# Performance work log

Hardware: AMD Instinct MI355X
Metric: run time of the kernel (lower is better)

The kernel has to match this reference:

```python
import jax, jax.numpy as jnp
import numpy as np

EPS = 1e-8

def setup_inputs() -> dict:
    key = jax.random.key(0)
    k1, k2 = jax.random.split(key)
    B, IN, OUT, G = 32768, 256, 256, 5
    x = jax.random.normal(k1, (B, IN), dtype=jnp.float32)
    grid = jnp.linspace(-1.0, 1.0, G).astype(jnp.float32)
    coef = jax.random.normal(k2, (OUT, IN, G), dtype=jnp.float32) * 0.1
    scale = jnp.ones((OUT, IN), dtype=jnp.float32)
    bias = jnp.zeros((OUT,), dtype=jnp.float32)
    return {"x": x, "grid": grid, "coef": coef, "scale": scale, "bias": bias}

def reference(x, grid, coef, scale, bias):
    # global min-max normalization to [-1, 1]
    xmin, xmax = x.min(), x.max()
    xn = 2.0 * (x - xmin) / (xmax - xmin + EPS) - 1.0
    # cubic bump B-spline-like basis: (batch, in, grid)
    dist = jnp.abs(xn[..., None] - grid)
    basis = jnp.where(dist < 1.0, 1.0 - dist ** 3, 0.0)
    basis = basis / (basis.sum(axis=-1, keepdims=True) + EPS)
    # fused contraction over (in, grid); equals ((basis*coef).sum(-1)*scale).sum(-1)
    w = coef * scale[..., None]          # (out, in, grid)
    out = jnp.einsum('big,oig->bo', basis, w) + bias
    return out
```

## Files before the change

### kernel.cpp

```cpp
#include <hip/hip_runtime.h>
#include <stdint.h>


#define B_SZ   32768
#define IN_SZ  256
#define OUT_SZ 256
#define EPSF   1e-8f

typedef __bf16 bf16x8 __attribute__((ext_vector_type(8)));
typedef unsigned short ushort8 __attribute__((ext_vector_type(8)));
typedef float floatx16 __attribute__((ext_vector_type(16)));

union frag_u { uint4 u; bf16x8 v; };

__device__ __forceinline__ unsigned short f2bf(float f) {
  unsigned u = __float_as_uint(f);
  u += 0x7FFFu + ((u >> 16) & 1u);
  return (unsigned short)(u >> 16);
}


__global__ void __launch_bounds__(256) prep_kernel(const float* __restrict__ coef,
                                                   const float* __restrict__ scale,
                                                   const float* __restrict__ x,
                                                   unsigned short* __restrict__ wf,
                                                   float* __restrict__ part, int n4) {
  const int t = threadIdx.x;
  if (blockIdx.x < 256) {
    int idx = blockIdx.x * 256 + t;
    int o = idx >> 8, i = idx & 255;
    float s = scale[idx];
    const float* c = coef + (size_t)idx * 5;
    ushort8 v;
    v[0] = f2bf(c[0] * s); v[1] = f2bf(c[1] * s); v[2] = f2bf(c[2] * s);
    v[3] = f2bf(c[3] * s); v[4] = f2bf(c[4] * s);
    v[5] = 0; v[6] = 0; v[7] = 0;
    int chunk = (((o >> 5) * 64 + (i >> 2)) * 2 + ((i >> 1) & 1)) * 64
                + (i & 1) * 32 + (o & 31);
    *(ushort8*)(wf + (size_t)chunk * 8) = v;
  } else {
    int mb = blockIdx.x - 256;
    const float4* x4 = (const float4*)x;
    float lmin = 1e30f, lmax = -1e30f;
    for (int i = mb * 256 + t; i < n4; i += 256 * 256) {
      float4 v = x4[i];
      lmin = fminf(lmin, fminf(fminf(v.x, v.y), fminf(v.z, v.w)));
      lmax = fmaxf(lmax, fmaxf(fmaxf(v.x, v.y), fmaxf(v.z, v.w)));
    }
    #pragma unroll
    for (int off = 32; off >= 1; off >>= 1) {
      lmin = fminf(lmin, __shfl_down(lmin, off, 64));
      lmax = fmaxf(lmax, __shfl_down(lmax, off, 64));
    }
    __shared__ float smn[4], smx[4];
    if ((t & 63) == 0) { smn[t >> 6] = lmin; smx[t >> 6] = lmax; }
    __syncthreads();
    if (t == 0) {
      part[2 * mb]     = fminf(fminf(smn[0], smn[1]), fminf(smn[2], smn[3]));
      part[2 * mb + 1] = fmaxf(fmaxf(smx[0], smx[1]), fmaxf(smx[2], smx[3]));
    }
  }
}

__device__ __forceinline__ bf16x8 basisfrag(float xval, float scA, float scB) {
  float xn = fmaf(xval, scA, scB);
  float d0 = xn + 1.0f, d1 = xn + 0.5f, d3 = xn - 0.5f, d4 = xn - 1.0f;
  float b0 = fmaxf(fmaf(d0 * d0, -fabsf(d0), 1.0f), 0.0f);
  float b1 = fmaxf(fmaf(d1 * d1, -fabsf(d1), 1.0f), 0.0f);
  float b2 = fmaxf(fmaf(xn * xn, -fabsf(xn), 1.0f), 0.0f);
  float b3 = fmaxf(fmaf(d3 * d3, -fabsf(d3), 1.0f), 0.0f);
  float b4 = fmaxf(fmaf(d4 * d4, -fabsf(d4), 1.0f), 0.0f);
  float sum = ((b0 + b1) + (b2 + b3)) + b4;
  float inv = __builtin_amdgcn_rcpf(sum);
  b0 *= inv; b1 *= inv; b2 *= inv; b3 *= inv; b4 *= inv;
  frag_u r;
  r.u.x = __builtin_amdgcn_perm(__float_as_uint(b1), __float_as_uint(b0), 0x07060302u);
  r.u.y = __builtin_amdgcn_perm(__float_as_uint(b3), __float_as_uint(b2), 0x07060302u);
  r.u.z = __float_as_uint(b4) >> 16;
  r.u.w = 0u;
  return r.v;
}

__global__ void __launch_bounds__(256, 2) kan_gemm(
    const float* __restrict__ x,
    const unsigned short* __restrict__ wf,
    const float* __restrict__ bias,
    const float* __restrict__ part,
    float* __restrict__ out)
{
  __shared__ __align__(16) unsigned short Bb[2][16384];
  __shared__ float2 red[4];

  const int t = threadIdx.x;
  const int lane = t & 63;
  const int wm = t >> 6;
  const int l31 = lane & 31, lh = lane >> 5;
  const int bRow = blockIdx.x * 128;
  const int bCol = blockIdx.y * 128;
  const int row = bRow + wm * 32 + l31;

  auto stage = [&](int c, int buf) {
    #pragma unroll
    for (int r = 0; r < 8; ++r) {
      int idx = r * 4 + wm;
      const unsigned short* src = wf +
          ((size_t)(((blockIdx.y * 4 + (idx >> 3)) * 64 + (c * 4 + ((idx >> 1) & 3))) * 2
                    + (idx & 1))) * 512 + (size_t)lane * 8;
      __builtin_amdgcn_global_load_lds(
          (const __attribute__((address_space(1))) unsigned int*)src,
          (__attribute__((address_space(3))) unsigned int*)(&Bb[buf][idx * 512 + lane * 8]),
          16, 0, 0);
    }
  };

  const float* xrow = x + (size_t)row * IN_SZ;

  stage(0, 0);
  float4 xq[4], xqn[4];
  #pragma unroll
  for (int g = 0; g < 4; ++g) xq[g] = *(const float4*)(xrow + g * 4);

  float2 p = ((const float2*)part)[t];
  float mn = p.x, mx = p.y;
  #pragma unroll
  for (int off = 32; off >= 1; off >>= 1) {
    mn = fminf(mn, __shfl_down(mn, off, 64));
    mx = fmaxf(mx, __shfl_down(mx, off, 64));
  }
  if (lane == 0) red[wm] = make_float2(mn, mx);
  __syncthreads();
  mn = fminf(fminf(red[0].x, red[1].x), fminf(red[2].x, red[3].x));
  mx = fmaxf(fmaxf(red[0].y, red[1].y), fmaxf(red[2].y, red[3].y));
  const float scA = 2.0f / (mx - mn + EPSF);
  const float scB = -mn * scA - 1.0f;

  floatx16 acc[4] = {};
  bf16x8 br[2][8];

  auto ldsB = [&](int ktr, int buf, bf16x8* dst) {
    #pragma unroll
    for (int q = 0; q < 8; ++q) {
      int ni = q >> 1, ks = q & 1;
      dst[q] = *(const bf16x8*)(&Bb[buf][((ni * 4 + ktr) * 2 + ks) * 512 + lane * 8]);
    }
  };

  for (int c = 0; c < 16; ++c) {
    const int buf = c & 1;

    if (c < 15) {
      #pragma unroll
      for (int g = 0; g < 4; ++g)
        xqn[g] = *(const float4*)(xrow + (c + 1) * 16 + g * 4);
      stage(c + 1, buf ^ 1);
      __builtin_amdgcn_sched_barrier(0);
      asm volatile("s_waitcnt vmcnt(12)\n\ts_barrier" ::: "memory");
    } else {
      asm volatile("s_waitcnt vmcnt(0)\n\ts_barrier" ::: "memory");
    }

    ldsB(0, buf, br[0]);

    #pragma unroll
    for (int ktr = 0; ktr < 4; ++ktr) {
      if (ktr < 3) ldsB(ktr + 1, buf, br[(ktr + 1) & 1]);

      float xv0 = lh ? xq[ktr].y : xq[ktr].x;
      float xv1 = lh ? xq[ktr].w : xq[ktr].z;
      bf16x8 af0 = basisfrag(xv0, scA, scB);
      bf16x8 af1 = basisfrag(xv1, scA, scB);

      bf16x8* B = br[ktr & 1];
      __builtin_amdgcn_s_setprio(1);
      #pragma unroll
      for (int ni = 0; ni < 4; ++ni)
        acc[ni] = __builtin_amdgcn_mfma_f32_32x32x16_bf16(af0, B[ni * 2 + 0], acc[ni], 0, 0, 0);
      #pragma unroll
      for (int ni = 0; ni < 4; ++ni)
        acc[ni] = __builtin_amdgcn_mfma_f32_32x32x16_bf16(af1, B[ni * 2 + 1], acc[ni], 0, 0, 0);
      __builtin_amdgcn_s_setprio(0);

      if (ktr < 3)
        __builtin_amdgcn_s_barrier();
    }

    if (c < 15) {
      asm volatile("s_waitcnt lgkmcnt(0)\n\ts_barrier" ::: "memory");
      #pragma unroll
      for (int g = 0; g < 4; ++g) xq[g] = xqn[g];
    }
  }

  #pragma unroll
  for (int ni = 0; ni < 4; ++ni) {
    int o = bCol + ni * 32 + l31;
    float bs = bias[o];
    int rb = bRow + wm * 32 + 4 * lh;
    #pragma unroll
    for (int reg = 0; reg < 16; ++reg) {
      int r = rb + (reg & 3) + 8 * (reg >> 2);
      out[(size_t)r * OUT_SZ + o] = acc[ni][reg] + bs;
    }
  }
}

extern "C" void kernel_launch(void* const* d_in, const int* in_sizes, int n_in,
                              void* d_out, int out_size, void* d_ws, size_t ws_size,
                              hipStream_t stream) {
  const float* x     = (const float*)d_in[0];
  const float* coef  = (const float*)d_in[2];
  const float* scale = (const float*)d_in[3];
  const float* bias  = (const float*)d_in[4];
  float* out = (float*)d_out;

  size_t need = 4096 + (size_t)OUT_SZ * IN_SZ * 8 * 2;
  if (ws_size < need) return;

  float* part = (float*)d_ws;
  unsigned short* wf = (unsigned short*)((char*)d_ws + 4096);

  prep_kernel<<<512, 256, 0, stream>>>(coef, scale, x, wf, part,
                                       (B_SZ * IN_SZ) / 4);
  dim3 g(B_SZ / 128, OUT_SZ / 128);
  kan_gemm<<<g, 256, 0, stream>>>(x, wf, bias, part, out);
}
```

Before: 136.7 us.

## Halve GEMM column tile to 64, raise occupancy, widen min-max reduction grid

Shrinks each GEMM block's output tile from 128x128 to 128x64, halving LDS staging and accumulator registers so launch bounds can request 4 blocks per CU, and doubling the grid. It drops the per-k-step barriers and simplifies the wait/barrier structure. The min-max reduction in the prep kernel now uses 1536 blocks instead of 256, so each GEMM block reduces 1536 partials instead of 256. Trade-offs: x is loaded and the basis recomputed twice as often per output, and each block does more partial-reduction work.

```diff
diff --git a/kernel.cpp b/kernel.cpp
--- a/kernel.cpp
+++ b/kernel.cpp
@@ -6,6 +6,7 @@
 #define IN_SZ  256
 #define OUT_SZ 256
 #define EPSF   1e-8f
+#define NMB    1536
 
 typedef __bf16 bf16x8 __attribute__((ext_vector_type(8)));
 typedef unsigned short ushort8 __attribute__((ext_vector_type(8)));
@@ -42,7 +43,7 @@
     int mb = blockIdx.x - 256;
     const float4* x4 = (const float4*)x;
     float lmin = 1e30f, lmax = -1e30f;
-    for (int i = mb * 256 + t; i < n4; i += 256 * 256) {
+    for (int i = mb * 256 + t; i < n4; i += NMB * 256) {
       float4 v = x4[i];
       lmin = fminf(lmin, fminf(fminf(v.x, v.y), fminf(v.z, v.w)));
       lmax = fmaxf(lmax, fmaxf(fmaxf(v.x, v.y), fmaxf(v.z, v.w)));
@@ -81,14 +82,14 @@
   return r.v;
 }
 
-__global__ void __launch_bounds__(256, 2) kan_gemm(
+__global__ void __launch_bounds__(256, 4) kan_gemm(
     const float* __restrict__ x,
     const unsigned short* __restrict__ wf,
     const float* __restrict__ bias,
     const float* __restrict__ part,
     float* __restrict__ out)
 {
-  __shared__ __align__(16) unsigned short Bb[2][16384];
+  __shared__ __align__(16) unsigned short Bb[2][8192];
   __shared__ float2 red[4];
 
   const int t = threadIdx.x;
@@ -96,15 +97,15 @@
   const int wm = t >> 6;
   const int l31 = lane & 31, lh = lane >> 5;
   const int bRow = blockIdx.x * 128;
-  const int bCol = blockIdx.y * 128;
+  const int bCol = blockIdx.y * 64;
   const int row = bRow + wm * 32 + l31;
 
   auto stage = [&](int c, int buf) {
     #pragma unroll
-    for (int r = 0; r < 8; ++r) {
+    for (int r = 0; r < 4; ++r) {
       int idx = r * 4 + wm;
       const unsigned short* src = wf +
-          ((size_t)(((blockIdx.y * 4 + (idx >> 3)) * 64 + (c * 4 + ((idx >> 1) & 3))) * 2
+          ((size_t)(((blockIdx.y * 2 + (idx >> 3)) * 64 + (c * 4 + ((idx >> 1) & 3))) * 2
                     + (idx & 1))) * 512 + (size_t)lane * 8;
       __builtin_amdgcn_global_load_lds(
           (const __attribute__((address_space(1))) unsigned int*)src,
@@ -120,8 +121,13 @@
   #pragma unroll
   for (int g = 0; g < 4; ++g) xq[g] = *(const float4*)(xrow + g * 4);
 
-  float2 p = ((const float2*)part)[t];
-  float mn = p.x, mx = p.y;
+  float mn = 1e30f, mx = -1e30f;
+  const float2* part2 = (const float2*)part;
+  #pragma unroll
+  for (int k = 0; k < NMB / 256; ++k) {
+    float2 p = part2[k * 256 + t];
+    mn = fminf(mn, p.x); mx = fmaxf(mx, p.y);
+  }
   #pragma unroll
   for (int off = 32; off >= 1; off >>= 1) {
     mn = fminf(mn, __shfl_down(mn, off, 64));
@@ -134,12 +140,12 @@
   const float scA = 2.0f / (mx - mn + EPSF);
   const float scB = -mn * scA - 1.0f;
 
-  floatx16 acc[4] = {};
-  bf16x8 br[2][8];
+  floatx16 acc[2] = {};
+  bf16x8 br[2][4];
 
   auto ldsB = [&](int ktr, int buf, bf16x8* dst) {
     #pragma unroll
-    for (int q = 0; q < 8; ++q) {
+    for (int q = 0; q < 4; ++q) {
       int ni = q >> 1, ks = q & 1;
       dst[q] = *(const bf16x8*)(&Bb[buf][((ni * 4 + ktr) * 2 + ks) * 512 + lane * 8]);
     }
@@ -153,11 +159,12 @@
       for (int g = 0; g < 4; ++g)
         xqn[g] = *(const float4*)(xrow + (c + 1) * 16 + g * 4);
       stage(c + 1, buf ^ 1);
-      __builtin_amdgcn_sched_barrier(0);
-      asm volatile("s_waitcnt vmcnt(12)\n\ts_barrier" ::: "memory");
-    } else {
-      asm volatile("s_waitcnt vmcnt(0)\n\ts_barrier" ::: "memory");
-    }
+    }
+    __builtin_amdgcn_sched_barrier(0);
+    if (c < 15) asm volatile("s_waitcnt vmcnt(8)");
+    else        asm volatile("s_waitcnt vmcnt(0)");
+    __builtin_amdgcn_s_barrier();
+    __builtin_amdgcn_sched_barrier(0);
 
     ldsB(0, buf, br[0]);
 
@@ -170,29 +177,26 @@
       bf16x8 af0 = basisfrag(xv0, scA, scB);
       bf16x8 af1 = basisfrag(xv1, scA, scB);
 
-      bf16x8* B = br[ktr & 1];
+      bf16x8* Bf = br[ktr & 1];
       __builtin_amdgcn_s_setprio(1);
-      #pragma unroll
-      for (int ni = 0; ni < 4; ++ni)
-        acc[ni] = __builtin_amdgcn_mfma_f32_32x32x16_bf16(af0, B[ni * 2 + 0], acc[ni], 0, 0, 0);
-      #pragma unroll
-      for (int ni = 0; ni < 4; ++ni)
-        acc[ni] = __builtin_amdgcn_mfma_f32_32x32x16_bf16(af1, B[ni * 2 + 1], acc[ni], 0, 0, 0);
+      acc[0] = __builtin_amdgcn_mfma_f32_32x32x16_bf16(af0, Bf[0], acc[0], 0, 0, 0);
+      acc[1] = __builtin_amdgcn_mfma_f32_32x32x16_bf16(af0, Bf[2], acc[1], 0, 0, 0);
+      acc[0] = __builtin_amdgcn_mfma_f32_32x32x16_bf16(af1, Bf[1], acc[0], 0, 0, 0);
+      acc[1] = __builtin_amdgcn_mfma_f32_32x32x16_bf16(af1, Bf[3], acc[1], 0, 0, 0);
       __builtin_amdgcn_s_setprio(0);
-
-      if (ktr < 3)
-        __builtin_amdgcn_s_barrier();
     }
 
     if (c < 15) {
-      asm volatile("s_waitcnt lgkmcnt(0)\n\ts_barrier" ::: "memory");
       #pragma unroll
       for (int g = 0; g < 4; ++g) xq[g] = xqn[g];
-    }
-  }
-
-  #pragma unroll
-  for (int ni = 0; ni < 4; ++ni) {
+      __builtin_amdgcn_sched_barrier(0);
+      __builtin_amdgcn_s_barrier();
+      __builtin_amdgcn_sched_barrier(0);
+    }
+  }
+
+  #pragma unroll
+  for (int ni = 0; ni < 2; ++ni) {
     int o = bCol + ni * 32 + l31;
     float bs = bias[o];
     int rb = bRow + wm * 32 + 4 * lh;
@@ -213,14 +217,14 @@
   const float* bias  = (const float*)d_in[4];
   float* out = (float*)d_out;
 
-  size_t need = 4096 + (size_t)OUT_SZ * IN_SZ * 8 * 2;
+  size_t need = 16384 + (size_t)OUT_SZ * IN_SZ * 8 * 2;
   if (ws_size < need) return;
 
   float* part = (float*)d_ws;
-  unsigned short* wf = (unsigned short*)((char*)d_ws + 4096);
-
-  prep_kernel<<<512, 256, 0, stream>>>(coef, scale, x, wf, part,
-                                       (B_SZ * IN_SZ) / 4);
-  dim3 g(B_SZ / 128, OUT_SZ / 128);
+  unsigned short* wf = (unsigned short*)((char*)d_ws + 16384);
+
+  prep_kernel<<<256 + NMB, 256, 0, stream>>>(coef, scale, x, wf, part,
+                                             (B_SZ * IN_SZ) / 4);
+  dim3 g(B_SZ / 128, OUT_SZ / 64);
   kan_gemm<<<g, 256, 0, stream>>>(x, wf, bias, part, out);
 }
```

New measurement: 142.1 us. +3.9%, slower.
